# Kernel tuning notes

Measured on AMD Instinct MI355X. Metric: run time of the kernel, lower is better.

## Reference

```python
import jax, jax.numpy as jnp
import numpy as np

DIM, HEADS, WS = 256, 16, 8
B, H, W = 2, 252, 252
BN_EPS = 1e-5


def _rel_index():
    # Same construction as the torch buffer relative_position_index (64,64)
    coords = np.stack(np.meshgrid(np.arange(WS), np.arange(WS), indexing='ij'))
    flat = coords.reshape(2, -1)
    rel = (flat[:, :, None] - flat[:, None, :]).transpose(1, 2, 0).copy()
    rel[..., 0] += WS - 1
    rel[..., 1] += WS - 1
    rel[..., 0] *= 2 * WS - 1
    return jnp.asarray(rel.sum(-1))

REL_IDX = _rel_index()  # (WS*WS, WS*WS) int


def _conv(x, w, pad, groups=1):
    return jax.lax.conv_general_dilated(
        x, w, (1, 1), [(pad[0], pad[0]), (pad[1], pad[1])],
        dimension_numbers=('NCHW', 'OIHW', 'NCHW'), feature_group_count=groups)


def setup_inputs() -> dict:
    key = jax.random.key(0)
    ks = jax.random.split(key, 8)
    s = lambda k, shape, sc: jax.random.normal(k, shape, jnp.float32) * sc
    z = lambda: jnp.zeros((DIM,), jnp.float32)
    return {
        'x': s(ks[0], (B, DIM, H, W), 1.0),
        'w_qkv': s(ks[1], (3 * DIM, DIM, 1, 1), 0.05),
        'rel_bias_table': s(ks[2], ((2 * WS - 1) ** 2, HEADS), 0.02),
        'w_h': s(ks[3], (DIM, DIM, WS, 1), 0.02),
        'b_h': z(),
        'w_v': s(ks[4], (DIM, DIM, 1, WS), 0.02),
        'b_v': z(),
        'w_dw': s(ks[5], (DIM, 1, WS, WS), 0.05),
        'bn_gamma': jnp.ones((DIM,), jnp.float32),
        'bn_beta': z(),
        'bn_mean': z(),
        'bn_var': jnp.ones((DIM,), jnp.float32),
        'w_pw': s(ks[6], (DIM, DIM, 1, 1), 0.05),
    }


def reference(x, w_qkv, rel_bias_table, w_h, b_h, w_v, b_v, w_dw,
              bn_gamma, bn_beta, bn_mean, bn_var, w_pw):
    Bc, C, Hc, Wc = x.shape
    pad_h, pad_w = WS - Hc % WS, WS - Wc % WS
    xp = jnp.pad(x, ((0, 0), (0, 0), (0, pad_h), (0, pad_w)), mode='reflect')
    Hp, Wp = Hc + pad_h, Wc + pad_w
    hh, ww, d = Hp // WS, Wp // WS, C // HEADS

    qkv = _conv(xp, w_qkv, (0, 0))  # (B, 3C, Hp, Wp)
    # b (qkv h d) (hh ws1) (ww ws2) -> qkv (b hh ww) h (ws1 ws2) d
    qkv = qkv.reshape(Bc, 3, HEADS, d, hh, WS, ww, WS)
    qkv = qkv.transpose(1, 0, 4, 6, 2, 5, 7, 3).reshape(3, Bc * hh * ww, HEADS, WS * WS, d)
    q, k, v = qkv[0], qkv[1], qkv[2]

    dots = jnp.einsum('nhid,nhjd->nhij', q, k) * (d ** -0.5)
    bias = rel_bias_table[REL_IDX.reshape(-1)].reshape(WS * WS, WS * WS, HEADS)
    dots = dots + bias.transpose(2, 0, 1)[None]  # (1, h, 64, 64)
    attn = jax.nn.softmax(dots, axis=-1)
    out = jnp.einsum('nhij,nhjd->nhid', attn, v)
    # (b hh ww) h (ws1 ws2) d -> b (h d) (hh ws1) (ww ws2)
    out = out.reshape(Bc, hh, ww, HEADS, WS, WS, d)
    out = out.transpose(0, 3, 6, 1, 4, 2, 5).reshape(Bc, C, Hp, Wp)
    out = out[:, :, :Hc, :Wc]

    p1 = _conv(jnp.pad(out, ((0, 0), (0, 0), (0, 1), (0, 0)), mode='reflect'),
               w_h, (WS // 2 - 1, 0)) + b_h[None, :, None, None]
    p2 = _conv(jnp.pad(out, ((0, 0), (0, 0), (0, 0), (0, 1)), mode='reflect'),
               w_v, (0, WS // 2 - 1)) + b_v[None, :, None, None]
    y = jnp.pad(p1 + p2, ((0, 0), (0, 0), (0, 1), (0, 1)), mode='reflect')
    y = _conv(y, w_dw, ((WS - 1) // 2, (WS - 1) // 2), groups=DIM)  # depthwise
    inv = bn_gamma / jnp.sqrt(bn_var + BN_EPS)
    y = y * inv[None, :, None, None] + (bn_beta - bn_mean * inv)[None, :, None, None]
    y = _conv(y, w_pw, (0, 0))  # pointwise 1x1
    return y[:, :, :Hc, :Wc]
```

## Files before the change

### kernel.cpp

```cpp
#include <hip/hip_runtime.h>
#include <hip/hip_bf16.h>

#define HC 252
#define WC 252
#define CD 256
#define NHEADS 16

#define XP_W 264
#define XP_ROW (XP_W*256)
#define XP_BH  (252*XP_ROW)

typedef unsigned short u16;
typedef unsigned int u32;
typedef __attribute__((ext_vector_type(8))) short bf16x8;
typedef __attribute__((ext_vector_type(4))) float f32x4;
typedef __attribute__((ext_vector_type(4))) u32 u32x4;
typedef __attribute__((ext_vector_type(2))) u32 u32x2;

#define XP_BYTES (2u * 2u * (unsigned)XP_BH)
#define ZP_OFF   XP_BYTES
#define ZP_BYTES 409600u
#define WT_OFF   (ZP_OFF + ZP_BYTES)
#define WT_ELEMS (128*8192)
#define WPW_OFF  (WT_OFF + (unsigned)WT_ELEMS*2u)
#define WPW_ELEMS (8*8192)
#define WQ_OFF   (WPW_OFF + (unsigned)WPW_ELEMS*2u)
#define WQ_ELEMS (768*256)
#define BIAS_OFF (WQ_OFF + (unsigned)WQ_ELEMS*2u)

__device__ __forceinline__ u16 bfu(float f) {
    __hip_bfloat16 h = __float2bfloat16(f);
    return *(reinterpret_cast<u16*>(&h));
}
__device__ __forceinline__ u32 pack2(float a, float b) {
    return (u32)bfu(a) | ((u32)bfu(b) << 16);
}
__device__ __forceinline__ float bf2f(u16 v) {
    union { u32 u; float f; } cv; cv.u = ((u32)v) << 16; return cv.f;
}

__global__ __launch_bounds__(256, 2) void attn_mfma(
    const float* __restrict__ x, const u16* __restrict__ WQ,
    const float* __restrict__ BIASF, u16* __restrict__ xp)
{
    __shared__ __align__(16) char smem[73728];

    const int bid = blockIdx.x;
    const int zz = (bid & 7) * 256 + (bid >> 3);
    const int wx = zz & 31, wy = (zz >> 5) & 31, b = zz >> 10;
    const int tid = threadIdx.x;
    const int lane = tid & 63, wid = tid >> 6;
    const int g = lane >> 4, li = lane & 15;

    {
        int ci = tid;
        const float* srcc = x + (size_t)(b * 256 + ci) * (HC * WC);
        #pragma unroll
        for (int r = 0; r < 8; ++r) {
            int h = wy * 8 + r; if (h >= HC) h = 2 * HC - 2 - h;
            const float* src = srcc + h * WC;
            float v[8];
            if (wx == 31) {
                #pragma unroll
                for (int c = 0; c < 8; ++c) {
                    int w = 248 + c; if (w >= WC) w = 2 * WC - 2 - w;
                    v[c] = src[w];
                }
            } else {
                float4 f0 = *(const float4*)(src + wx * 8);
                float4 f1 = *(const float4*)(src + wx * 8 + 4);
                v[0]=f0.x; v[1]=f0.y; v[2]=f0.z; v[3]=f0.w;
                v[4]=f1.x; v[5]=f1.y; v[6]=f1.z; v[7]=f1.w;
            }
            #pragma unroll
            for (int c = 0; c < 8; ++c) {
                int pos = r * 8 + c;
                int byte = pos * 512 + ((ci * 2) ^ ((pos & 7) << 4));
                *(u16*)(smem + byte) = bfu(v[c]);
            }
        }
    }
    __syncthreads();

    const int WB = 32768 + wid * 10240;
    char* Qb = smem + WB;
    char* Kb = smem + WB + 2048;
    char* Vb = smem + WB + 4096;
    char* Pb = smem + WB + 6144;

    const bf16x8 zf = {0,0,0,0,0,0,0,0};

    #pragma unroll 1
    for (int hh = 0; hh < 4; ++hh) {
        const int head = wid * 4 + hh;

        f32x4 acc[3][4];
        #pragma unroll
        for (int p = 0; p < 3; ++p)
            #pragma unroll
            for (int nf = 0; nf < 4; ++nf) acc[p][nf] = (f32x4){0.f,0.f,0.f,0.f};

        for (int ks = 0; ks < 8; ++ks) {
            bf16x8 bx[4];
            #pragma unroll
            for (int nf = 0; nf < 4; ++nf) {
                int pos = 16 * nf + li;
                int byte = pos * 512 + ((ks * 64 + 16 * g) ^ ((pos & 7) << 4));
                bx[nf] = *(const bf16x8*)(smem + byte);
            }
            bf16x8 aw[3];
            #pragma unroll
            for (int p = 0; p < 3; ++p) {
                int o = p * 256 + head * 16 + li;
                aw[p] = *(const bf16x8*)(WQ + o * 256 + ks * 32 + 8 * g);
            }
            __builtin_amdgcn_s_setprio(1);
            #pragma unroll
            for (int p = 0; p < 3; ++p)
                #pragma unroll
                for (int nf = 0; nf < 4; ++nf)
                    acc[p][nf] = __builtin_amdgcn_mfma_f32_16x16x32_bf16(aw[p], bx[nf], acc[p][nf], 0, 0, 0);
            __builtin_amdgcn_s_setprio(0);
        }

        #pragma unroll
        for (int p = 0; p < 3; ++p) {
            if (p < 2) {
                char* base = (p == 0) ? Qb : Kb;
                #pragma unroll
                for (int nf = 0; nf < 4; ++nf) {
                    int pos = 16 * nf + li;
                    u32 lo = pack2(acc[p][nf][0], acc[p][nf][1]);
                    u32 hi = pack2(acc[p][nf][2], acc[p][nf][3]);
                    int byte = pos * 32 + ((8 * g) ^ (((pos >> 2) & 1) << 4));
                    *(u32x2*)(base + byte) = (u32x2){lo, hi};
                }
            } else {
                #pragma unroll
                for (int nf = 0; nf < 4; ++nf) {
                    int pos = 16 * nf + li;
                    #pragma unroll
                    for (int r = 0; r < 4; ++r) {
                        int d = 4 * g + r;
                        int byte = (pos >> 3) * 256 + d * 16 + (pos & 7) * 2;
                        *(u16*)(Vb + byte) = bfu(acc[p][nf][r]);
                    }
                }
            }
        }

        f32x4 s[4][4];
        #pragma unroll
        for (int mf = 0; mf < 4; ++mf)
            #pragma unroll
            for (int nf = 0; nf < 4; ++nf) s[mf][nf] = (f32x4){0.f,0.f,0.f,0.f};
        bf16x8 bk[4];
        #pragma unroll
        for (int nf = 0; nf < 4; ++nf) {
            int pos = 16 * nf + li;
            bk[nf] = (g < 2) ? *(const bf16x8*)(Kb + pos * 32 + ((16 * g) ^ (((pos >> 2) & 1) << 4))) : zf;
        }
        __builtin_amdgcn_s_setprio(1);
        #pragma unroll
        for (int mf = 0; mf < 4; ++mf) {
            int pos = 16 * mf + li;
            bf16x8 aq = (g < 2) ? *(const bf16x8*)(Qb + pos * 32 + ((16 * g) ^ (((pos >> 2) & 1) << 4))) : zf;
            #pragma unroll
            for (int nf = 0; nf < 4; ++nf)
                s[mf][nf] = __builtin_amdgcn_mfma_f32_16x16x32_bf16(aq, bk[nf], s[mf][nf], 0, 0, 0);
        }
        __builtin_amdgcn_s_setprio(0);

        f32x4 e[4][4];
        f32x4 rs[4];
        #pragma unroll
        for (int mf = 0; mf < 4; ++mf) rs[mf] = (f32x4){0.f,0.f,0.f,0.f};
        #pragma unroll
        for (int mf = 0; mf < 4; ++mf)
            #pragma unroll
            for (int nf = 0; nf < 4; ++nf) {
                f32x4 b4 = *(const f32x4*)(BIASF + (((head * 4 + mf) * 4 + nf) * 64 + lane) * 4);
                #pragma unroll
                for (int r = 0; r < 4; ++r) {
                    float ev = __expf(s[mf][nf][r] * 0.25f + b4[r]);
                    e[mf][nf][r] = ev;
                    rs[mf][r] += ev;
                }
            }
        #pragma unroll
        for (int mf = 0; mf < 4; ++mf)
            #pragma unroll
            for (int r = 0; r < 4; ++r) {
                float t = rs[mf][r];
                t += __shfl_xor(t, 1); t += __shfl_xor(t, 2);
                t += __shfl_xor(t, 4); t += __shfl_xor(t, 8);
                rs[mf][r] = t;
            }

        f32x4 o[4];
        #pragma unroll
        for (int mf = 0; mf < 4; ++mf) o[mf] = (f32x4){0.f,0.f,0.f,0.f};
        const bool even = !(lane & 1);
        #pragma unroll
        for (int hf = 0; hf < 2; ++hf) {
            #pragma unroll
            for (int mf = 0; mf < 4; ++mf)
                #pragma unroll
                for (int nfl = 0; nfl < 2; ++nfl) {
                    f32x4 ee = e[mf][2 * hf + nfl];
                    float p0 = __shfl_xor(ee[0], 1), p1 = __shfl_xor(ee[1], 1);
                    float p2 = __shfl_xor(ee[2], 1), p3 = __shfl_xor(ee[3], 1);
                    int jl = 16 * nfl + (li & ~1);
                    u32 w0, w1; int r0;
                    if (even) { w0 = pack2(ee[0], p0); w1 = pack2(ee[1], p1); r0 = 0; }
                    else      { w0 = pack2(p2, ee[2]); w1 = pack2(p3, ee[3]); r0 = 2; }
                    int i0 = 16 * mf + 4 * g + r0, i1 = i0 + 1;
                    *(u32*)(Pb + i0 * 64 + ((2 * jl) ^ ((i0 & 3) << 4))) = w0;
                    *(u32*)(Pb + i1 * 64 + ((2 * jl) ^ ((i1 & 3) << 4))) = w1;
                }
            bf16x8 bv = *(const bf16x8*)(Vb + (4 * hf + g) * 256 + li * 16);
            __builtin_amdgcn_s_setprio(1);
            #pragma unroll
            for (int mf = 0; mf < 4; ++mf) {
                int i = 16 * mf + li;
                bf16x8 ap = *(const bf16x8*)(Pb + i * 64 + ((16 * g) ^ ((i & 3) << 4)));
                o[mf] = __builtin_amdgcn_mfma_f32_16x16x32_bf16(ap, bv, o[mf], 0, 0, 0);
            }
            __builtin_amdgcn_s_setprio(0);
        }

        #pragma unroll
        for (int mf = 0; mf < 4; ++mf) {
            int h = wy * 8 + 2 * mf + (g >> 1);
            int wbase = wx * 8 + 4 * (g & 1);
            if (h < HC && wbase < WC) {
                size_t rowb = ((size_t)(b * HC + h)) * XP_ROW + (size_t)(head * 16 + li);
                #pragma unroll
                for (int r = 0; r < 4; ++r) {
                    float v = o[mf][r] / rs[mf][r];
                    xp[rowb + (size_t)(wbase + r + 4) * 256] = bfu(v);
                }
            }
        }
    }
}

__global__ __launch_bounds__(256) void wprep_kernel(
    const float* __restrict__ wh, const float* __restrict__ wv,
    const float* __restrict__ wpw, const float* __restrict__ wqkv,
    const float* __restrict__ btab, u16* __restrict__ wsu)
{
    int i = blockIdx.x * 256 + threadIdx.x;
    u16* WT = wsu + WT_OFF / 2;
    u16* WP = wsu + WPW_OFF / 2;
    u16* ZP = wsu + ZP_OFF / 2;
    u16* WQp = wsu + WQ_OFF / 2;
    float* BF = (float*)(wsu + BIAS_OFF / 2);
    if (i < WT_ELEMS) {
        int j = i & 7, l = (i >> 3) & 1023, s = i >> 13;
        int kb = (l >> 8) & 3;
        int co = (l & 255) ^ (kb << 1);
        float v;
        if (s < 64) {
            int t = s >> 3, ci = (s & 7) * 32 + kb * 8 + j;
            v = wh[co * 2048 + ci * 8 + t];
        } else {
            int s2 = s - 64;
            int t = s2 >> 3, ci = (s2 & 7) * 32 + kb * 8 + j;
            v = wv[co * 2048 + ci * 8 + t];
        }
        WT[i] = bfu(v);
    } else if (i < WT_ELEMS + WPW_ELEMS) {
        int i2 = i - WT_ELEMS;
        int j = i2 & 7, l = (i2 >> 3) & 1023, s = i2 >> 13;
        int kb = (l >> 8) & 3;
        int co = (l & 255) ^ (kb << 1);
        WP[i2] = bfu(wpw[co * 256 + s * 32 + kb * 8 + j]);
    } else if (i < WT_ELEMS + WPW_ELEMS + (int)(ZP_BYTES / 2)) {
        ZP[i - WT_ELEMS - WPW_ELEMS] = 0;
    } else if (i < WT_ELEMS + WPW_ELEMS + (int)(ZP_BYTES / 2) + WQ_ELEMS) {
        int i4 = i - WT_ELEMS - WPW_ELEMS - (int)(ZP_BYTES / 2);
        WQp[i4] = bfu(wqkv[i4]);
    } else {
        int i5 = i - WT_ELEMS - WPW_ELEMS - (int)(ZP_BYTES / 2) - WQ_ELEMS;
        if (i5 < 16384) {
            int lane = i5 & 63, nf = (i5 >> 6) & 3, mf = (i5 >> 8) & 3, head = i5 >> 10;
            int gg = lane >> 4, ll = lane & 15;
            #pragma unroll
            for (int r = 0; r < 4; ++r) {
                int row = 16 * mf + 4 * gg + r;
                int col = 16 * nf + ll;
                int dy = (row >> 3) - (col >> 3) + 7;
                int dx = (row & 7) - (col & 7) + 7;
                BF[i5 * 4 + r] = btab[(dy * 15 + dx) * NHEADS + head];
            }
        }
    }
}

__global__ __launch_bounds__(256) void halo_kernel(u16* __restrict__ xp)
{
    int i = blockIdx.x * 256 + threadIdx.x;
    if (i >= 2 * 252 * 12 * 256) return;
    int ci = i & 255;
    int c12 = (i >> 8) % 12;
    int row = i / (12 * 256);
    int wp = (c12 < 4) ? c12 : 252 + c12;
    u16 v = 0;
    if (wp == 256) v = xp[(size_t)row * XP_ROW + 254 * 256 + ci];
    xp[(size_t)row * XP_ROW + (size_t)wp * 256 + ci] = v;
}

__global__ __launch_bounds__(512, 2) void sepconv_mfma(
    const u16* __restrict__ xpt, const u16* __restrict__ WT,
    const u16* __restrict__ ZP,
    const float* __restrict__ b_h, const float* __restrict__ b_v,
    u16* __restrict__ P)
{
    __shared__ __align__(16) u16 As[2][8192];
    __shared__ __align__(16) u16 Bs[2][256 * 36];

    const int bid = blockIdx.x;
    const int zz = (bid & 7) * 63 + (bid >> 3);
    const int h = zz % HC, b = zz / HC;
    const int tid = threadIdx.x;
    const int lane = tid & 63, wid = tid >> 6;
    const int wr = wid >> 2, wc = wid & 3;
    const int cq = lane & 15, kb = lane >> 4;

    const int wB = tid & 255;
    const int oc0 = tid >> 8;
    const int tb = (wB + 4) * 256 + oc0 * 8;
    const int bsw = wB * 36 + oc0 * 8;

    const u16* const xb = xpt + (size_t)(b * HC) * XP_ROW;

    f32x4 acc[8][4];
    #pragma unroll
    for (int m = 0; m < 8; ++m)
        #pragma unroll
        for (int n = 0; n < 4; ++n) acc[m][n] = (f32x4){0.f, 0.f, 0.f, 0.f};

    u32x4 rA[2];
    u32x4 rB0, rB1;

#define SC_SRC(t, RP, SO)                                                      \
    if ((t) < 64) {                                                            \
        int tt = (t) >> 3;                                                     \
        int jt = h + tt - 3;                                                   \
        int jr = (jt == 252) ? 250 : jt;                                       \
        RP = (jt >= 0 && jt <= 252) ? (xpt + ((size_t)(b * HC) + jr) * XP_ROW) : ZP; \
        SO = ((t) & 7) * 32;                                                   \
    } else {                                                                   \
        int tt = ((t) - 64) >> 3;                                              \
        RP = xb + (size_t)h * XP_ROW + (tt - 3) * 256;                         \
        SO = (((t) - 64) & 7) * 32;                                            \
    }

    rA[0] = *(const u32x4*)(WT + (size_t)tid * 8);
    rA[1] = *(const u32x4*)(WT + (size_t)(512 + tid) * 8);
    {
        const u16* rp; int so;
        SC_SRC(0, rp, so)
        rB0 = *(const u32x4*)(rp + so + tb);
        rB1 = *(const u32x4*)(rp + so + tb + 16);
    }
    *(u32x4*)&As[0][(size_t)tid * 8] = rA[0];
    *(u32x4*)&As[0][(size_t)(512 + tid) * 8] = rA[1];
    *(u32x4*)&Bs[0][bsw] = rB0;
    *(u32x4*)&Bs[0][bsw + 16] = rB1;

    #pragma unroll 1
    for (int s = 0; s < 128; ++s) {
        const int cur = s & 1;
        const int s1 = s + 1;
        if (s1 < 128) {
            rA[0] = *(const u32x4*)(WT + (size_t)s1 * 8192 + (size_t)tid * 8);
            rA[1] = *(const u32x4*)(WT + (size_t)s1 * 8192 + (size_t)(512 + tid) * 8);
            const u16* rp; int so;
            SC_SRC(s1, rp, so)
            rB0 = *(const u32x4*)(rp + so + tb);
            rB1 = *(const u32x4*)(rp + so + tb + 16);
        }
        __syncthreads();

        {
            bf16x8 af[8], bfr[4];
            #pragma unroll
            for (int m = 0; m < 8; ++m) {
                int row = wr * 128 + m * 16 + cq;
                af[m] = *(const bf16x8*)&As[cur][(kb * 256 + (row ^ (kb << 1))) * 8];
            }
            #pragma unroll
            for (int n = 0; n < 4; ++n)
                bfr[n] = *(const bf16x8*)&Bs[cur][(wc * 64 + n * 16 + cq) * 36 + kb * 8];
            __builtin_amdgcn_s_setprio(1);
            #pragma unroll
            for (int m = 0; m < 8; ++m)
                #pragma unroll
                for (int n = 0; n < 4; ++n)
                    acc[m][n] = __builtin_amdgcn_mfma_f32_16x16x32_bf16(af[m], bfr[n], acc[m][n], 0, 0, 0);
            __builtin_amdgcn_s_setprio(0);
        }

        if (s1 < 128) {
            const int nxt = cur ^ 1;
            *(u32x4*)&As[nxt][(size_t)tid * 8] = rA[0];
            *(u32x4*)&As[nxt][(size_t)(512 + tid) * 8] = rA[1];
            *(u32x4*)&Bs[nxt][bsw] = rB0;
            *(u32x4*)&Bs[nxt][bsw + 16] = rB1;
        }
    }
#undef SC_SRC

    const int rq = lane >> 4, cc = lane & 15;
    #pragma unroll
    for (int m = 0; m < 8; ++m) {
        int cgb = wr * 128 + m * 16 + rq * 4;
        float bias[4];
        #pragma unroll
        for (int rr = 0; rr < 4; ++rr) bias[rr] = b_h[cgb + rr] + b_v[cgb + rr];
        #pragma unroll
        for (int n = 0; n < 4; ++n) {
            int wg = wc * 64 + n * 16 + cc;
            if (wg < WC) {
                #pragma unroll
                for (int rr = 0; rr < 4; ++rr)
                    P[((size_t)(b * CD + cgb + rr) * HC + h) * WC + wg] = bfu(acc[m][n][rr] + bias[rr]);
            }
        }
    }
}

__global__ __launch_bounds__(256) void dwbn_kernel(
    const u16* __restrict__ P, const float* __restrict__ w_dw,
    const float* __restrict__ gamma, const float* __restrict__ beta,
    const float* __restrict__ mean, const float* __restrict__ var,
    __hip_bfloat16* __restrict__ Yb)
{
    __shared__ float ps[15][42];
    __shared__ float wd[64];
    const int bw = blockIdx.x, bh = blockIdx.y, bz = blockIdx.z;
    const int b = bz >> 8, c = bz & 255;
    const int h0 = bh * 8, w0 = bw * 32;
    const int tid = threadIdx.x;
    if (tid < 64) wd[tid] = w_dw[c * 64 + tid];
    for (int it = 0; it < 3; ++it) {
        int flat = tid + it * 256;
        if (flat < 630) {
            int row = flat / 42, col = flat % 42;
            int j = h0 - 3 + row, wcol = w0 - 3 + col;
            float v = 0.f;
            if (j >= 0 && j <= HC && wcol >= 0 && wcol <= WC) {
                int jr = (j == HC) ? (HC - 2) : j;
                int wr2 = (wcol == WC) ? (WC - 2) : wcol;
                v = bf2f(P[((size_t)(b * CD + c) * HC + jr) * WC + wr2]);
            }
            ps[row][col] = v;
        }
    }
    __syncthreads();
    const int r = tid >> 5, cc = tid & 31;
    const int h = h0 + r, w = w0 + cc;
    if (h < HC && w < WC) {
        float s = 0.f;
        #pragma unroll
        for (int u = 0; u < 8; ++u)
            #pragma unroll
            for (int v2 = 0; v2 < 8; ++v2)
                s += wd[u * 8 + v2] * ps[r + u][cc + v2];
        const float inv = gamma[c] * rsqrtf(var[c] + 1e-5f);
        Yb[((b * CD + c) * HC + h) * WC + w] = __float2bfloat16(s * inv + (beta[c] - mean[c] * inv));
    }
}

__global__ __launch_bounds__(512, 2) void pw_mfma(
    const u16* __restrict__ Y, const u16* __restrict__ WP,
    float* __restrict__ O)
{
    __shared__ __align__(16) u16 As[2][8192];
    __shared__ __align__(16) u16 Bs[2][256 * 36];

    const int bid = blockIdx.x;
    const int zz = (bid & 7) * 63 + (bid >> 3);
    const int h = zz % HC, b = zz / HC;
    const int tid = threadIdx.x;
    const int lane = tid & 63, wid = tid >> 6;
    const int wr = wid >> 2, wc = wid & 3;
    const int cq = lane & 15, kb = lane >> 4;

    const int wl2 = (tid & 127) * 2;
    const int oc = tid >> 7;

    const u16* yb = Y + ((size_t)(b * 256 + oc * 8) * HC + h) * WC + wl2;

    const int bw0 = wl2 * 36 + oc * 8;
    const int bw1 = bw0 + 36;

    f32x4 acc[8][4];
    #pragma unroll
    for (int m = 0; m < 8; ++m)
        #pragma unroll
        for (int n = 0; n < 4; ++n) acc[m][n] = (f32x4){0.f, 0.f, 0.f, 0.f};

    u32x4 rA[2];
    u32 rB[8];

    rA[0] = *(const u32x4*)(WP + (size_t)tid * 8);
    rA[1] = *(const u32x4*)(WP + (size_t)(512 + tid) * 8);
    #pragma unroll
    for (int j = 0; j < 8; ++j)
        rB[j] = *(const u32*)(yb + (size_t)j * (HC * WC));
    *(u32x4*)&As[0][(size_t)tid * 8] = rA[0];
    *(u32x4*)&As[0][(size_t)(512 + tid) * 8] = rA[1];
    {
        union { bf16x8 v; u32 u[4]; } p0, p1;
        #pragma unroll
        for (int q = 0; q < 4; ++q) {
            p0.u[q] = __builtin_amdgcn_perm(rB[2 * q + 1], rB[2 * q], 0x05040100u);
            p1.u[q] = __builtin_amdgcn_perm(rB[2 * q + 1], rB[2 * q], 0x07060302u);
        }
        *(bf16x8*)&Bs[0][bw0] = p0.v;
        *(bf16x8*)&Bs[0][bw1] = p1.v;
    }

    #pragma unroll 1
    for (int s = 0; s < 8; ++s) {
        const int cur = s & 1;
        const int s1 = s + 1;
        if (s1 < 8) {
            rA[0] = *(const u32x4*)(WP + (size_t)s1 * 8192 + (size_t)tid * 8);
            rA[1] = *(const u32x4*)(WP + (size_t)s1 * 8192 + (size_t)(512 + tid) * 8);
            #pragma unroll
            for (int j = 0; j < 8; ++j)
                rB[j] = *(const u32*)(yb + (size_t)(s1 * 32 + j) * (HC * WC));
        }
        __syncthreads();

        {
            bf16x8 af[8], bfr[4];
            #pragma unroll
            for (int m = 0; m < 8; ++m) {
                int row = wr * 128 + m * 16 + cq;
                af[m] = *(const bf16x8*)&As[cur][(kb * 256 + (row ^ (kb << 1))) * 8];
            }
            #pragma unroll
            for (int n = 0; n < 4; ++n)
                bfr[n] = *(const bf16x8*)&Bs[cur][(wc * 64 + n * 16 + cq) * 36 + kb * 8];
            __builtin_amdgcn_s_setprio(1);
            #pragma unroll
            for (int m = 0; m < 8; ++m)
                #pragma unroll
                for (int n = 0; n < 4; ++n)
                    acc[m][n] = __builtin_amdgcn_mfma_f32_16x16x32_bf16(af[m], bfr[n], acc[m][n], 0, 0, 0);
            __builtin_amdgcn_s_setprio(0);
        }

        if (s1 < 8) {
            const int nxt = cur ^ 1;
            *(u32x4*)&As[nxt][(size_t)tid * 8] = rA[0];
            *(u32x4*)&As[nxt][(size_t)(512 + tid) * 8] = rA[1];
            union { bf16x8 v; u32 u[4]; } p0, p1;
            #pragma unroll
            for (int q = 0; q < 4; ++q) {
                p0.u[q] = __builtin_amdgcn_perm(rB[2 * q + 1], rB[2 * q], 0x05040100u);
                p1.u[q] = __builtin_amdgcn_perm(rB[2 * q + 1], rB[2 * q], 0x07060302u);
            }
            *(bf16x8*)&Bs[nxt][bw0] = p0.v;
            *(bf16x8*)&Bs[nxt][bw1] = p1.v;
        }
    }

    const int rq = lane >> 4, cc = lane & 15;
    #pragma unroll
    for (int m = 0; m < 8; ++m) {
        int cgb = wr * 128 + m * 16 + rq * 4;
        #pragma unroll
        for (int n = 0; n < 4; ++n) {
            int wg = wc * 64 + n * 16 + cc;
            if (wg < WC) {
                #pragma unroll
                for (int rr = 0; rr < 4; ++rr)
                    O[((size_t)(b * CD + cgb + rr) * HC + h) * WC + wg] = acc[m][n][rr];
            }
        }
    }
}

extern "C" void kernel_launch(void* const* d_in, const int* in_sizes, int n_in,
                              void* d_out, int out_size, void* d_ws, size_t ws_size,
                              hipStream_t stream)
{
    const float* x      = (const float*)d_in[0];
    const float* w_qkv  = (const float*)d_in[1];
    const float* bias_t = (const float*)d_in[2];
    const float* w_h    = (const float*)d_in[3];
    const float* b_h    = (const float*)d_in[4];
    const float* w_v    = (const float*)d_in[5];
    const float* b_v    = (const float*)d_in[6];
    const float* w_dw   = (const float*)d_in[7];
    const float* bn_g   = (const float*)d_in[8];
    const float* bn_b   = (const float*)d_in[9];
    const float* bn_m   = (const float*)d_in[10];
    const float* bn_v   = (const float*)d_in[11];
    const float* w_pw   = (const float*)d_in[12];
    float* out = (float*)d_out;

    u16* wsu = (u16*)d_ws;
    const u16* XPu = wsu;
    const u16* ZPu = wsu + ZP_OFF / 2;
    const u16* WTu = wsu + WT_OFF / 2;
    const u16* WPu = wsu + WPW_OFF / 2;
    const u16* WQu = wsu + WQ_OFF / 2;
    const float* BFu = (const float*)(wsu + BIAS_OFF / 2);

    wprep_kernel<<<5984, 256, 0, stream>>>(w_h, w_v, w_pw, w_qkv, bias_t, wsu);
    attn_mfma<<<2048, 256, 0, stream>>>(x, WQu, BFu, wsu);
    halo_kernel<<<6048, 256, 0, stream>>>(wsu);
    sepconv_mfma<<<504, 512, 0, stream>>>(XPu, WTu, ZPu, b_h, b_v, (u16*)d_out);
    dwbn_kernel<<<dim3(8, 32, 512), 256, 0, stream>>>((const u16*)d_out, w_dw, bn_g, bn_b,
                                                      bn_m, bn_v, (__hip_bfloat16*)d_ws);
    pw_mfma<<<504, 512, 0, stream>>>(wsu, WPu, out);
}
```

Before: 689.6 us.

## Load separable-conv B fragments directly from global into registers, drop LDS staging

The B operand (shifted input rows) of the separable-conv MFMA GEMM is now loaded straight from global memory into per-wave register fragments instead of being staged through a padded LDS buffer. The main loop is unrolled by two with ping-pong register sets (bA/bB), and the A weights are still double-buffered in LDS. This removes the LDS writes and reads for B and halves LDS use, which may allow better occupancy. In exchange, each wave issues redundant global loads for B (the four wr/wc wave groups reread overlapping data) and register pressure rises.

```diff
diff --git a/kernel.cpp b/kernel.cpp
--- a/kernel.cpp
+++ b/kernel.cpp
@@ -318,7 +318,6 @@
     u16* __restrict__ P)
 {
     __shared__ __align__(16) u16 As[2][8192];
-    __shared__ __align__(16) u16 Bs[2][256 * 36];
 
     const int bid = blockIdx.x;
     const int zz = (bid & 7) * 63 + (bid >> 3);
@@ -328,12 +327,8 @@
     const int wr = wid >> 2, wc = wid & 3;
     const int cq = lane & 15, kb = lane >> 4;
 
-    const int wB = tid & 255;
-    const int oc0 = tid >> 8;
-    const int tb = (wB + 4) * 256 + oc0 * 8;
-    const int bsw = wB * 36 + oc0 * 8;
-
     const u16* const xb = xpt + (size_t)(b * HC) * XP_ROW;
+    const int fragb = (wc * 64 + cq + 4) * 256 + kb * 8;
 
     f32x4 acc[8][4];
     #pragma unroll
@@ -342,7 +337,7 @@
         for (int n = 0; n < 4; ++n) acc[m][n] = (f32x4){0.f, 0.f, 0.f, 0.f};
 
     u32x4 rA[2];
-    u32x4 rB0, rB1;
+    u32x4 bA[4], bB[4];
 
 #define SC_SRC(t, RP, SO)                                                      \
     if ((t) < 64) {                                                            \
@@ -357,61 +352,65 @@
         SO = (((t) - 64) & 7) * 32;                                            \
     }
 
-    rA[0] = *(const u32x4*)(WT + (size_t)tid * 8);
-    rA[1] = *(const u32x4*)(WT + (size_t)(512 + tid) * 8);
-    {
-        const u16* rp; int so;
-        SC_SRC(0, rp, so)
-        rB0 = *(const u32x4*)(rp + so + tb);
-        rB1 = *(const u32x4*)(rp + so + tb + 16);
-    }
-    *(u32x4*)&As[0][(size_t)tid * 8] = rA[0];
-    *(u32x4*)&As[0][(size_t)(512 + tid) * 8] = rA[1];
-    *(u32x4*)&Bs[0][bsw] = rB0;
-    *(u32x4*)&Bs[0][bsw + 16] = rB1;
+#define SC_LOADA(t)                                                            \
+    if ((t) < 128) {                                                           \
+        rA[0] = *(const u32x4*)(WT + (size_t)(t) * 8192 + (size_t)tid * 8);    \
+        rA[1] = *(const u32x4*)(WT + (size_t)(t) * 8192 + (size_t)(512 + tid) * 8); \
+    }
+
+#define SC_LOADB(t, BD)                                                        \
+    if ((t) < 128) {                                                           \
+        const u16* rp_; int so_;                                               \
+        SC_SRC(t, rp_, so_)                                                    \
+        _Pragma("unroll") for (int n = 0; n < 4; ++n)                          \
+            BD[n] = *(const u32x4*)(rp_ + so_ + fragb + n * (16 * 256));       \
+    }
+
+#define SC_WRITEA(t, buf)                                                      \
+    if ((t) < 128) {                                                           \
+        *(u32x4*)&As[buf][(size_t)tid * 8] = rA[0];                            \
+        *(u32x4*)&As[buf][(size_t)(512 + tid) * 8] = rA[1];                    \
+    }
+
+#define SC_MFMA(buf, BD)                                                       \
+    {                                                                          \
+        bf16x8 af[8];                                                          \
+        _Pragma("unroll") for (int m = 0; m < 8; ++m) {                        \
+            int row_ = wr * 128 + m * 16 + cq;                                 \
+            af[m] = *(const bf16x8*)&As[buf][(kb * 256 + (row_ ^ (kb << 1))) * 8]; \
+        }                                                                      \
+        __builtin_amdgcn_s_setprio(1);                                         \
+        _Pragma("unroll") for (int m = 0; m < 8; ++m) {                        \
+            _Pragma("unroll") for (int n = 0; n < 4; ++n)                      \
+                acc[m][n] = __builtin_amdgcn_mfma_f32_16x16x32_bf16(af[m], *(const bf16x8*)&BD[n], acc[m][n], 0, 0, 0); \
+        }                                                                      \
+        __builtin_amdgcn_s_setprio(0);                                         \
+    }
+
+    SC_LOADA(0)
+    SC_LOADB(0, bA)
+    SC_WRITEA(0, 0)
+    SC_LOADA(1)
 
     #pragma unroll 1
-    for (int s = 0; s < 128; ++s) {
-        const int cur = s & 1;
-        const int s1 = s + 1;
-        if (s1 < 128) {
-            rA[0] = *(const u32x4*)(WT + (size_t)s1 * 8192 + (size_t)tid * 8);
-            rA[1] = *(const u32x4*)(WT + (size_t)s1 * 8192 + (size_t)(512 + tid) * 8);
-            const u16* rp; int so;
-            SC_SRC(s1, rp, so)
-            rB0 = *(const u32x4*)(rp + so + tb);
-            rB1 = *(const u32x4*)(rp + so + tb + 16);
-        }
+    for (int sb = 0; sb < 128; sb += 2) {
+        SC_LOADB(sb + 1, bB)
         __syncthreads();
-
-        {
-            bf16x8 af[8], bfr[4];
-            #pragma unroll
-            for (int m = 0; m < 8; ++m) {
-                int row = wr * 128 + m * 16 + cq;
-                af[m] = *(const bf16x8*)&As[cur][(kb * 256 + (row ^ (kb << 1))) * 8];
-            }
-            #pragma unroll
-            for (int n = 0; n < 4; ++n)
-                bfr[n] = *(const bf16x8*)&Bs[cur][(wc * 64 + n * 16 + cq) * 36 + kb * 8];
-            __builtin_amdgcn_s_setprio(1);
-            #pragma unroll
-            for (int m = 0; m < 8; ++m)
-                #pragma unroll
-                for (int n = 0; n < 4; ++n)
-                    acc[m][n] = __builtin_amdgcn_mfma_f32_16x16x32_bf16(af[m], bfr[n], acc[m][n], 0, 0, 0);
-            __builtin_amdgcn_s_setprio(0);
-        }
-
-        if (s1 < 128) {
-            const int nxt = cur ^ 1;
-            *(u32x4*)&As[nxt][(size_t)tid * 8] = rA[0];
-            *(u32x4*)&As[nxt][(size_t)(512 + tid) * 8] = rA[1];
-            *(u32x4*)&Bs[nxt][bsw] = rB0;
-            *(u32x4*)&Bs[nxt][bsw + 16] = rB1;
-        }
-    }
+        SC_MFMA(0, bA)
+        SC_WRITEA(sb + 1, 1)
+        SC_LOADA(sb + 2)
+        SC_LOADB(sb + 2, bA)
+        __syncthreads();
+        SC_MFMA(1, bB)
+        SC_WRITEA(sb + 2, 0)
+        SC_LOADA(sb + 3)
+    }
+
 #undef SC_SRC
+#undef SC_LOADA
+#undef SC_LOADB
+#undef SC_WRITEA
+#undef SC_MFMA
 
     const int rq = lane >> 4, cc = lane & 15;
     #pragma unroll
```

Result: slower. 714.5 us (+3.6%).
